# Performance work log

Hardware: AMD Instinct MI355X
Metric: run time of the kernel (lower is better)

## Reference

```python
import jax, jax.numpy as jnp
import numpy as np

D_IN = 2048
D_OUT = 2048
LN_EPS = 1e-5


def setup_inputs() -> dict:
    key = jax.random.key(0)
    kx, kw, kb = jax.random.split(key, 3)
    x = jax.random.normal(kx, (8, 2048, D_IN), dtype=jnp.float32)
    # LayerNorm affine params (torch defaults: ones / zeros)
    gamma = jnp.ones((D_IN,), dtype=jnp.float32)
    beta = jnp.zeros((D_IN,), dtype=jnp.float32)
    # weight = rand(out,in)*0.001, bias = rand(out)*0.001, alpha = ones(out)
    weight = jax.random.uniform(kw, (D_OUT, D_IN), dtype=jnp.float32) * 0.001
    bias = jax.random.uniform(kb, (D_OUT,), dtype=jnp.float32) * 0.001
    alpha = jnp.ones((D_OUT,), dtype=jnp.float32)
    return {"x": x, "gamma": gamma, "beta": beta, "weight": weight,
            "bias": bias, "alpha": alpha}


def reference(x, gamma, beta, weight, bias, alpha):
    # LayerNorm over last dim (biased variance, eps=1e-5, affine)
    mu = jnp.mean(x, axis=-1, keepdims=True)
    var = jnp.mean(jnp.square(x - mu), axis=-1, keepdims=True)
    xn = (x - mu) * jax.lax.rsqrt(var + LN_EPS) * gamma + beta
    # Binarize activations: hard sign
    a = jnp.sign(xn)
    # Binarize weights: mean-center per output row, clip, sign (STE in fwd == sign)
    centered = weight - jnp.mean(weight, axis=1, keepdims=True)  # [O, I]
    signed_w = jnp.sign(centered)
    # Linear + bias, then per-output-channel alpha scale
    out = jnp.einsum('bsi,oi->bso', a, signed_w) + bias
    return out * alpha
```

## Files before the change

kernel.cpp:

```cpp
#include <hip/hip_runtime.h>

#define DIN 2048
#define WPR 64
#define QPR 32
#define GPR 16
#define RPB 8
#define LN_EPS 1e-5f

#define GLOBAL_AS __attribute__((address_space(1)))
#define LDS_AS    __attribute__((address_space(3)))

typedef unsigned long long u64;
typedef int   i32x4  __attribute__((ext_vector_type(4)));
typedef int   i32x8  __attribute__((ext_vector_type(8)));
typedef float f32x16 __attribute__((ext_vector_type(16)));

__device__ inline float wave_sum(float v) {
    #pragma unroll
    for (int off = 32; off; off >>= 1) v += __shfl_down(v, off, 64);
    return v;
}


__global__ __launch_bounds__(256) void expand_kernel(const float* __restrict__ x,
                                                     const float* __restrict__ gamma,
                                                     const float* __restrict__ beta,
                                                     const float* __restrict__ w,
                                                     char* __restrict__ Aexp,
                                                     char* __restrict__ Bexp,
                                                     int Mblocks) {
    const int t = threadIdx.x;
    const int wid = t >> 6, lane = t & 63;
    __shared__ float red[4][2 * RPB];
    __shared__ __align__(16) unsigned stg[RPB * 256];

    const bool isA = (int)blockIdx.x < Mblocks;
    const int r0 = (isA ? (int)blockIdx.x : ((int)blockIdx.x - Mblocks)) * RPB;
    const float* src = isA ? x : w;

    float gg[8], bb[8];
    if (isA) {
        float4 g0 = ((const float4*)gamma)[t * 2];
        float4 g1 = ((const float4*)gamma)[t * 2 + 1];
        float4 b0 = ((const float4*)beta)[t * 2];
        float4 b1 = ((const float4*)beta)[t * 2 + 1];
        gg[0]=g0.x; gg[1]=g0.y; gg[2]=g0.z; gg[3]=g0.w;
        gg[4]=g1.x; gg[5]=g1.y; gg[6]=g1.z; gg[7]=g1.w;
        bb[0]=b0.x; bb[1]=b0.y; bb[2]=b0.z; bb[3]=b0.w;
        bb[4]=b1.x; bb[5]=b1.y; bb[6]=b1.z; bb[7]=b1.w;
    }

    float vv[RPB][8];
    #pragma unroll
    for (int rr = 0; rr < RPB; ++rr) {
        const float* xr = src + (size_t)(r0 + rr) * DIN;
        float4 v0 = ((const float4*)xr)[t * 2];
        float4 v1 = ((const float4*)xr)[t * 2 + 1];
        vv[rr][0]=v0.x; vv[rr][1]=v0.y; vv[rr][2]=v0.z; vv[rr][3]=v0.w;
        vv[rr][4]=v1.x; vv[rr][5]=v1.y; vv[rr][6]=v1.z; vv[rr][7]=v1.w;
    }

    #pragma unroll
    for (int rr = 0; rr < RPB; ++rr) {
        float s = 0.f, ss = 0.f;
        #pragma unroll
        for (int j = 0; j < 8; ++j) s += vv[rr][j];
        if (isA) {
            #pragma unroll
            for (int j = 0; j < 8; ++j) ss += vv[rr][j] * vv[rr][j];
        }
        s = wave_sum(s);
        if (isA) ss = wave_sum(ss);
        if (lane == 0) { red[wid][rr * 2] = s; red[wid][rr * 2 + 1] = ss; }
    }
    __syncthreads();

    #pragma unroll
    for (int rr = 0; rr < RPB; ++rr) {
        float tot = red[0][rr*2] + red[1][rr*2] + red[2][rr*2] + red[3][rr*2];
        float mu  = tot * (1.f / DIN);
        unsigned word = 0;
        if (isA) {
            float tots = red[0][rr*2+1] + red[1][rr*2+1] + red[2][rr*2+1] + red[3][rr*2+1];
            float var  = tots * (1.f / DIN) - mu * mu;
            float rs   = rsqrtf(var + LN_EPS);
            #pragma unroll
            for (int j = 0; j < 8; ++j) {
                float xn = (vv[rr][j] - mu) * rs * gg[j] + bb[j];
                word |= (xn < 0.f ? 0xAu : 0x2u) << (4 * j);
            }
        } else {
            #pragma unroll
            for (int j = 0; j < 8; ++j)
                word |= ((vv[rr][j] - mu) < 0.f ? 0xAu : 0x2u) << (4 * j);
        }
        stg[rr * 256 + (((t >> 2) ^ rr) << 2) + (t & 3)] = word;
    }
    __syncthreads();

    char* dstbase = isA ? Aexp : Bexp;
    const int bm  = r0 >> 8;
    const int rt  = (r0 >> 5) & 7;
    const int ri0 = r0 & 31;
    #pragma unroll
    for (int i2 = 0; i2 < 2; ++i2) {
        const int u  = i2 * 256 + t;
        const int sc = u >> 5;
        const int kt = (u >> 4) & 1, hb = (u >> 3) & 1, ri = u & 7;
        const int g  = sc * 4 + kt * 2 + hb;
        uint4 v = *(const uint4*)&stg[ri * 256 + ((g ^ ri) << 2)];
        const size_t doff = (((size_t)(bm * 16 + sc)) * 8 + rt) * 2048 + kt * 1024 +
                            (ri0 + ri + 32 * hb) * 16;
        *(uint4*)(dstbase + doff) = v;
    }
}

__global__ __launch_bounds__(512, 4) void fp4gemm_kernel(const char* __restrict__ Aexp,
                                                         const char* __restrict__ Bexp,
                                                         const float* __restrict__ bias,
                                                         const float* __restrict__ alpha,
                                                         float* __restrict__ out) {
    __shared__ char As[2][8192];
    __shared__ char Bs[2][16384];
    const int t = threadIdx.x;
    const int wid = t >> 6, lane = t & 63;
    const int bn = blockIdx.x & 7;
    const int bm = blockIdx.x >> 3;
    const int wr = wid >> 2;
    const int wc = wid & 3;

    const char* gA = Aexp + (size_t)(bm >> 1) * 262144 + (size_t)(bm & 1) * 8192;
    const char* gB = Bexp + (size_t)bn * 262144;

#define STAGE(BUF, S)                                                           \
    {                                                                           \
        __builtin_amdgcn_global_load_lds(                                       \
            (const GLOBAL_AS unsigned*)(gA + (size_t)(S) * 16384 + wid * 1024 + lane * 16), \
            (LDS_AS unsigned*)(&As[BUF][wid * 1024]), 16, 0, 0);                \
        __builtin_amdgcn_global_load_lds(                                       \
            (const GLOBAL_AS unsigned*)(gB + (size_t)(S) * 16384 + wid * 1024 + lane * 16), \
            (LDS_AS unsigned*)(&Bs[BUF][wid * 1024]), 16, 0, 0);                \
        __builtin_amdgcn_global_load_lds(                                       \
            (const GLOBAL_AS unsigned*)(gB + (size_t)(S) * 16384 + (wid + 8) * 1024 + lane * 16), \
            (LDS_AS unsigned*)(&Bs[BUF][(wid + 8) * 1024]), 16, 0, 0);          \
    }

    f32x16 acc[2][2];
    #pragma unroll
    for (int i = 0; i < 2; ++i)
        #pragma unroll
        for (int j = 0; j < 2; ++j)
            #pragma unroll
            for (int e = 0; e < 16; ++e) acc[i][j][e] = 0.f;

    STAGE(0, 0)
    STAGE(1, 1)
    asm volatile("s_waitcnt vmcnt(3)" ::: "memory");
    __builtin_amdgcn_s_barrier();
    asm volatile("" ::: "memory");

    #pragma unroll 1
    for (int s = 0; s < 16; ++s) {
        const int c = s & 1;
        #pragma unroll
        for (int kt = 0; kt < 2; ++kt) {
            i32x8 a[2], b[2];
            #pragma unroll
            for (int i = 0; i < 2; ++i) {
                i32x4 v = *(const i32x4*)&As[c][(wr * 2 + i) * 2048 + kt * 1024 + lane * 16];
                a[i][0]=v[0]; a[i][1]=v[1]; a[i][2]=v[2]; a[i][3]=v[3];
                a[i][4]=v[0]; a[i][5]=v[1]; a[i][6]=v[2]; a[i][7]=v[3];
            }
            #pragma unroll
            for (int j = 0; j < 2; ++j) {
                i32x4 v = *(const i32x4*)&Bs[c][(wc * 2 + j) * 2048 + kt * 1024 + lane * 16];
                b[j][0]=v[0]; b[j][1]=v[1]; b[j][2]=v[2]; b[j][3]=v[3];
                b[j][4]=v[0]; b[j][5]=v[1]; b[j][6]=v[2]; b[j][7]=v[3];
            }
            __builtin_amdgcn_s_setprio(1);
            #pragma unroll
            for (int i = 0; i < 2; ++i)
                #pragma unroll
                for (int j = 0; j < 2; ++j)
                    acc[i][j] = __builtin_amdgcn_mfma_scale_f32_32x32x64_f8f6f4(
                        a[i], b[j], acc[i][j], 4, 4,
                        0, 0x7F7F7F7F, 0, 0x7F7F7F7F);
            __builtin_amdgcn_s_setprio(0);
        }
        if (s == 15) break;
        asm volatile("s_waitcnt vmcnt(0)" ::: "memory");
        __builtin_amdgcn_s_barrier();
        asm volatile("" ::: "memory");
        if (s < 14) STAGE(c, s + 2)
    }
#undef STAGE

    const int cl = lane & 31;
    const int rb = 4 * (lane >> 5);
    #pragma unroll
    for (int i = 0; i < 2; ++i) {
        #pragma unroll
        for (int j = 0; j < 2; ++j) {
            const int col = bn * 256 + (wc * 2 + j) * 32 + cl;
            const float bi = bias[col], al = alpha[col];
            const int row0 = bm * 128 + (wr * 2 + i) * 32 + rb;
            #pragma unroll
            for (int reg = 0; reg < 16; ++reg) {
                const int row = row0 + (reg & 3) + 8 * (reg >> 2);
                out[(size_t)row * 2048 + col] = (acc[i][j][reg] + bi) * al;
            }
        }
    }
}

__global__ __launch_bounds__(256) void w_pack_kernel(const float* __restrict__ w,
                                                     unsigned* __restrict__ wpk) {
    const int row = blockIdx.x;
    const int t = threadIdx.x;
    const float* wr = w + (size_t)row * DIN;
    float4 v0 = ((const float4*)wr)[t * 2];
    float4 v1 = ((const float4*)wr)[t * 2 + 1];
    float s = v0.x + v0.y + v0.z + v0.w + v1.x + v1.y + v1.z + v1.w;

    __shared__ float red[4];
    float wsum = wave_sum(s);
    int wid = t >> 6, lane = t & 63;
    if (lane == 0) red[wid] = wsum;
    __syncthreads();
    float mu = (red[0] + red[1] + red[2] + red[3]) * (1.f / DIN);

    float vv[8] = {v0.x, v0.y, v0.z, v0.w, v1.x, v1.y, v1.z, v1.w};
    unsigned byte = 0;
    #pragma unroll
    for (int j = 0; j < 8; ++j)
        byte |= ((vv[j] - mu) < 0.f ? 1u : 0u) << j;

    __shared__ unsigned char bytes[256];
    bytes[t] = (unsigned char)byte;
    __syncthreads();
    if (t < 64) {
        unsigned wd = (unsigned)bytes[t * 4] | ((unsigned)bytes[t * 4 + 1] << 8) |
                      ((unsigned)bytes[t * 4 + 2] << 16) | ((unsigned)bytes[t * 4 + 3] << 24);
        wpk[(size_t)row * WPR + t] = wd;
    }
}

__global__ __launch_bounds__(256) void ln_pack_kernel(const float* __restrict__ x,
                                                      const float* __restrict__ gamma,
                                                      const float* __restrict__ beta,
                                                      unsigned* __restrict__ apk) {
    const int row = blockIdx.x;
    const int t = threadIdx.x;
    const float* xr = x + (size_t)row * DIN;
    float4 v0 = ((const float4*)xr)[t * 2];
    float4 v1 = ((const float4*)xr)[t * 2 + 1];
    float s  = v0.x + v0.y + v0.z + v0.w + v1.x + v1.y + v1.z + v1.w;
    float ss = v0.x * v0.x + v0.y * v0.y + v0.z * v0.z + v0.w * v0.w +
               v1.x * v1.x + v1.y * v1.y + v1.z * v1.z + v1.w * v1.w;

    __shared__ float red[8];
    float wsum = wave_sum(s), wssum = wave_sum(ss);
    int wid = t >> 6, lane = t & 63;
    if (lane == 0) { red[wid] = wsum; red[4 + wid] = wssum; }
    __syncthreads();
    float tot  = red[0] + red[1] + red[2] + red[3];
    float tots = red[4] + red[5] + red[6] + red[7];
    float mu  = tot * (1.f / DIN);
    float var = tots * (1.f / DIN) - mu * mu;
    float rs  = rsqrtf(var + LN_EPS);

    float4 g0 = ((const float4*)gamma)[t * 2];
    float4 g1 = ((const float4*)gamma)[t * 2 + 1];
    float4 b0 = ((const float4*)beta)[t * 2];
    float4 b1 = ((const float4*)beta)[t * 2 + 1];
    float vv[8] = {v0.x, v0.y, v0.z, v0.w, v1.x, v1.y, v1.z, v1.w};
    float gg[8] = {g0.x, g0.y, g0.z, g0.w, g1.x, g1.y, g1.z, g1.w};
    float bb[8] = {b0.x, b0.y, b0.z, b0.w, b1.x, b1.y, b1.z, b1.w};
    unsigned byte = 0;
    #pragma unroll
    for (int j = 0; j < 8; ++j) {
        float xn = (vv[j] - mu) * rs * gg[j] + bb[j];
        byte |= (xn < 0.f ? 1u : 0u) << j;
    }

    __shared__ unsigned char bytes[256];
    bytes[t] = (unsigned char)byte;
    __syncthreads();
    if (t < 64) {
        unsigned wd = (unsigned)bytes[t * 4] | ((unsigned)bytes[t * 4 + 1] << 8) |
                      ((unsigned)bytes[t * 4 + 2] << 16) | ((unsigned)bytes[t * 4 + 3] << 24);
        apk[(size_t)row * WPR + t] = wd;
    }
}

__global__ __launch_bounds__(256) void bingemm_kernel(const u64* __restrict__ A,
                                                      const u64* __restrict__ B,
                                                      const float* __restrict__ bias,
                                                      const float* __restrict__ alpha,
                                                      float* __restrict__ out) {
    __shared__ u64 S[2 * 128 * QPR];
    uint4* Sg = (uint4*)S;
    const int t = threadIdx.x;
    const int bn = blockIdx.x, bm = blockIdx.y;

    const uint4* Ag = (const uint4*)(A + (size_t)bm * 128 * QPR);
    #pragma unroll
    for (int i = 0; i < 8; ++i) {
        int id = t + i * 256;
        int row = id >> 4, g = id & 15;
        Sg[(row << 4) + (g ^ (row & 15))] = Ag[id];
    }
    const uint4* Bg = (const uint4*)(B + (size_t)bn * 128 * QPR);
    #pragma unroll
    for (int i = 0; i < 8; ++i) {
        int id = t + i * 256;
        int row = id >> 4, g = id & 15;
        Sg[2048 + (row << 4) + (g ^ (row & 15))] = Bg[id];
    }
    __syncthreads();

    const int tr = t >> 4;
    const int tc = t & 15;
    const ulonglong2* Sq = (const ulonglong2*)S;
    const int abase = tr * GPR;
    const int bbase = 2048 + tc * GPR;

    int acc[8][8] = {};
    u64 a0[8][2], b0[8][2], a1[8][2], b1[8][2];

#define LOADK(KK, AR, BR)                                            \
    {                                                                \
        const int ka = abase + ((KK) ^ tr);                          \
        const int kb = bbase + ((KK) ^ tc);                          \
        _Pragma("unroll")                                            \
        for (int r = 0; r < 8; ++r) {                                \
            ulonglong2 v = Sq[ka + r * 256];                         \
            AR[r][0] = v.x; AR[r][1] = v.y;                          \
        }                                                            \
        _Pragma("unroll")                                            \
        for (int c2 = 0; c2 < 8; ++c2) {                             \
            ulonglong2 v = Sq[kb + c2 * 256];                        \
            BR[c2][0] = v.x; BR[c2][1] = v.y;                        \
        }                                                            \
    }

#define COMPK(AR, BR)                                                \
    {                                                                \
        _Pragma("unroll")                                            \
        for (int r = 0; r < 8; ++r) {                                \
            _Pragma("unroll")                                        \
            for (int c2 = 0; c2 < 8; ++c2) {                         \
                acc[r][c2] += __popcll(AR[r][0] ^ BR[c2][0]);        \
                acc[r][c2] += __popcll(AR[r][1] ^ BR[c2][1]);        \
            }                                                        \
        }                                                            \
    }

    LOADK(0, a0, b0);
    #pragma unroll 1
    for (int kk = 0; kk < 14; kk += 2) {
        LOADK(kk + 1, a1, b1);
        COMPK(a0, b0);
        LOADK(kk + 2, a0, b0);
        COMPK(a1, b1);
    }
    LOADK(15, a1, b1);
    COMPK(a0, b0);
    COMPK(a1, b1);
#undef LOADK
#undef COMPK

    float bi[8], al[8];
    #pragma unroll
    for (int c2 = 0; c2 < 8; ++c2) {
        int col = bn * 128 + tc + 16 * c2;
        bi[c2] = bias[col];
        al[c2] = alpha[col];
    }
    #pragma unroll
    for (int r = 0; r < 8; ++r) {
        const size_t row = (size_t)bm * 128 + tr + 16 * r;
        float* op = out + row * 2048 + bn * 128 + tc;
        #pragma unroll
        for (int c2 = 0; c2 < 8; ++c2)
            op[16 * c2] = ((float)(DIN - 2 * acc[r][c2]) + bi[c2]) * al[c2];
    }
}

extern "C" void kernel_launch(void* const* d_in, const int* in_sizes, int n_in,
                              void* d_out, int out_size, void* d_ws, size_t ws_size,
                              hipStream_t stream) {
    const float* x     = (const float*)d_in[0];
    const float* gamma = (const float*)d_in[1];
    const float* beta  = (const float*)d_in[2];
    const float* w     = (const float*)d_in[3];
    const float* bias  = (const float*)d_in[4];
    const float* alpha = (const float*)d_in[5];
    float* out = (float*)d_out;

    const int M = in_sizes[0] / DIN;
    const int N = in_sizes[3] / DIN;

    const size_t needA = (size_t)M * (DIN / 2);
    const size_t needB = (size_t)N * (DIN / 2);

    if (ws_size >= needA + needB && (M % 256) == 0 && (N % 256) == 0) {
        char* Aexp = (char*)d_ws;
        char* Bexp = (char*)d_ws + needA;
        expand_kernel<<<(M + N) / RPB, 256, 0, stream>>>(x, gamma, beta, w,
                                                         Aexp, Bexp, M / RPB);
        dim3 grid((N / 256) * (M / 128));
        fp4gemm_kernel<<<grid, 512, 0, stream>>>(Aexp, Bexp, bias, alpha, out);
    } else {
        unsigned* apk = (unsigned*)d_ws;
        unsigned* wpk = (unsigned*)((char*)d_ws + (size_t)M * WPR * 4);
        w_pack_kernel<<<N, 256, 0, stream>>>(w, wpk);
        ln_pack_kernel<<<M, 256, 0, stream>>>(x, gamma, beta, apk);
        dim3 grid(N / 128, M / 128);
        bingemm_kernel<<<grid, 256, 0, stream>>>((const u64*)apk, (const u64*)wpk,
                                                 bias, alpha, out);
    }
}
```

Baseline: 89.65 us.

## Load GEMM fragments directly into registers with double buffering, dropping LDS staging

```diff
diff --git a/kernel.cpp b/kernel.cpp
--- a/kernel.cpp
+++ b/kernel.cpp
@@ -115,99 +115,105 @@
     }
 }
 
-__global__ __launch_bounds__(512, 4) void fp4gemm_kernel(const char* __restrict__ Aexp,
+__global__ __launch_bounds__(256, 2) void fp4gemm_kernel(const char* __restrict__ Aexp,
                                                          const char* __restrict__ Bexp,
                                                          const float* __restrict__ bias,
                                                          const float* __restrict__ alpha,
-                                                         float* __restrict__ out) {
-    __shared__ char As[2][8192];
-    __shared__ char Bs[2][16384];
+                                                         float* __restrict__ out,
+                                                         int ldc, int nRb, int nCg) {
     const int t = threadIdx.x;
-    const int wid = t >> 6, lane = t & 63;
-    const int bn = blockIdx.x & 7;
-    const int bm = blockIdx.x >> 3;
-    const int wr = wid >> 2;
-    const int wc = wid & 3;
-
-    const char* gA = Aexp + (size_t)(bm >> 1) * 262144 + (size_t)(bm & 1) * 8192;
-    const char* gB = Bexp + (size_t)bn * 262144;
-
-#define STAGE(BUF, S)                                                           \
-    {                                                                           \
-        __builtin_amdgcn_global_load_lds(                                       \
-            (const GLOBAL_AS unsigned*)(gA + (size_t)(S) * 16384 + wid * 1024 + lane * 16), \
-            (LDS_AS unsigned*)(&As[BUF][wid * 1024]), 16, 0, 0);                \
-        __builtin_amdgcn_global_load_lds(                                       \
-            (const GLOBAL_AS unsigned*)(gB + (size_t)(S) * 16384 + wid * 1024 + lane * 16), \
-            (LDS_AS unsigned*)(&Bs[BUF][wid * 1024]), 16, 0, 0);                \
-        __builtin_amdgcn_global_load_lds(                                       \
-            (const GLOBAL_AS unsigned*)(gB + (size_t)(S) * 16384 + (wid + 8) * 1024 + lane * 16), \
-            (LDS_AS unsigned*)(&Bs[BUF][(wid + 8) * 1024]), 16, 0, 0);          \
-    }
-
-    f32x16 acc[2][2];
-    #pragma unroll
-    for (int i = 0; i < 2; ++i)
+    const int wv = t >> 6, lane = t & 63;
+    const int bid = blockIdx.x;
+    const int q = bid >> 3;
+    const int hi = q / nRb;
+    const int blockR = q - hi * nRb;
+    const int blockC = (bid & 7) * nCg + hi;
+
+    const int wr = wv >> 1, wc = wv & 1;
+    const int r128 = blockR * 2 + wr;
+    const int c64  = blockC * 2 + wc;
+    const int bm = r128 >> 1, rtbase = (r128 & 1) * 4;
+    const int bn = c64 >> 2,  ctbase = (c64 & 3) * 2;
+
+    const char* aP = Aexp + (size_t)bm * 262144 + (size_t)rtbase * 2048 + lane * 16;
+    const char* bP = Bexp + (size_t)bn * 262144 + (size_t)ctbase * 2048 + lane * 16;
+
+#define LOADP(P, AR, BR)                                                     \
+    {                                                                        \
+        const size_t off = (size_t)(((P) >> 1) * 16384 + ((P) & 1) * 1024);  \
+        _Pragma("unroll")                                                    \
+        for (int i = 0; i < 4; ++i)                                          \
+            AR[i] = *(const i32x4*)(aP + off + i * 2048);                    \
+        _Pragma("unroll")                                                    \
+        for (int j = 0; j < 2; ++j)                                          \
+            BR[j] = *(const i32x4*)(bP + off + j * 2048);                    \
+    }
+
+#define COMP(AR, BR)                                                         \
+    {                                                                        \
+        i32x8 aa[4], bb2[2];                                                 \
+        _Pragma("unroll")                                                    \
+        for (int i = 0; i < 4; ++i) {                                        \
+            aa[i][0]=AR[i][0]; aa[i][1]=AR[i][1];                            \
+            aa[i][2]=AR[i][2]; aa[i][3]=AR[i][3];                            \
+            aa[i][4]=AR[i][0]; aa[i][5]=AR[i][1];                            \
+            aa[i][6]=AR[i][2]; aa[i][7]=AR[i][3];                            \
+        }                                                                    \
+        _Pragma("unroll")                                                    \
+        for (int j = 0; j < 2; ++j) {                                        \
+            bb2[j][0]=BR[j][0]; bb2[j][1]=BR[j][1];                          \
+            bb2[j][2]=BR[j][2]; bb2[j][3]=BR[j][3];                          \
+            bb2[j][4]=BR[j][0]; bb2[j][5]=BR[j][1];                          \
+            bb2[j][6]=BR[j][2]; bb2[j][7]=BR[j][3];                          \
+        }                                                                    \
+        __builtin_amdgcn_s_setprio(1);                                       \
+        _Pragma("unroll")                                                    \
+        for (int i = 0; i < 4; ++i)                                          \
+            _Pragma("unroll")                                                \
+            for (int j = 0; j < 2; ++j)                                      \
+                acc[i][j] = __builtin_amdgcn_mfma_scale_f32_32x32x64_f8f6f4( \
+                    aa[i], bb2[j], acc[i][j], 4, 4,                          \
+                    0, 0x7F7F7F7F, 0, 0x7F7F7F7F);                           \
+        __builtin_amdgcn_s_setprio(0);                                       \
+    }
+
+    f32x16 acc[4][2];
+    #pragma unroll
+    for (int i = 0; i < 4; ++i)
         #pragma unroll
         for (int j = 0; j < 2; ++j)
             #pragma unroll
             for (int e = 0; e < 16; ++e) acc[i][j][e] = 0.f;
 
-    STAGE(0, 0)
-    STAGE(1, 1)
-    asm volatile("s_waitcnt vmcnt(3)" ::: "memory");
-    __builtin_amdgcn_s_barrier();
-    asm volatile("" ::: "memory");
-
+    i32x4 a0[4], b0[2], a1[4], b1[2];
+
+    LOADP(0, a0, b0);
     #pragma unroll 1
-    for (int s = 0; s < 16; ++s) {
-        const int c = s & 1;
-        #pragma unroll
-        for (int kt = 0; kt < 2; ++kt) {
-            i32x8 a[2], b[2];
-            #pragma unroll
-            for (int i = 0; i < 2; ++i) {
-                i32x4 v = *(const i32x4*)&As[c][(wr * 2 + i) * 2048 + kt * 1024 + lane * 16];
-                a[i][0]=v[0]; a[i][1]=v[1]; a[i][2]=v[2]; a[i][3]=v[3];
-                a[i][4]=v[0]; a[i][5]=v[1]; a[i][6]=v[2]; a[i][7]=v[3];
-            }
-            #pragma unroll
-            for (int j = 0; j < 2; ++j) {
-                i32x4 v = *(const i32x4*)&Bs[c][(wc * 2 + j) * 2048 + kt * 1024 + lane * 16];
-                b[j][0]=v[0]; b[j][1]=v[1]; b[j][2]=v[2]; b[j][3]=v[3];
-                b[j][4]=v[0]; b[j][5]=v[1]; b[j][6]=v[2]; b[j][7]=v[3];
-            }
-            __builtin_amdgcn_s_setprio(1);
-            #pragma unroll
-            for (int i = 0; i < 2; ++i)
-                #pragma unroll
-                for (int j = 0; j < 2; ++j)
-                    acc[i][j] = __builtin_amdgcn_mfma_scale_f32_32x32x64_f8f6f4(
-                        a[i], b[j], acc[i][j], 4, 4,
-                        0, 0x7F7F7F7F, 0, 0x7F7F7F7F);
-            __builtin_amdgcn_s_setprio(0);
-        }
-        if (s == 15) break;
-        asm volatile("s_waitcnt vmcnt(0)" ::: "memory");
-        __builtin_amdgcn_s_barrier();
-        asm volatile("" ::: "memory");
-        if (s < 14) STAGE(c, s + 2)
-    }
-#undef STAGE
+    for (int p = 0; p < 30; p += 2) {
+        LOADP(p + 1, a1, b1);
+        COMP(a0, b0);
+        LOADP(p + 2, a0, b0);
+        COMP(a1, b1);
+    }
+    LOADP(31, a1, b1);
+    COMP(a0, b0);
+    COMP(a1, b1);
+#undef LOADP
+#undef COMP
 
     const int cl = lane & 31;
     const int rb = 4 * (lane >> 5);
     #pragma unroll
-    for (int i = 0; i < 2; ++i) {
+    for (int i = 0; i < 4; ++i) {
         #pragma unroll
         for (int j = 0; j < 2; ++j) {
-            const int col = bn * 256 + (wc * 2 + j) * 32 + cl;
+            const int col = bn * 256 + (ctbase + j) * 32 + cl;
             const float bi = bias[col], al = alpha[col];
-            const int row0 = bm * 128 + (wr * 2 + i) * 32 + rb;
+            const int row0 = bm * 256 + (rtbase + i) * 32 + rb;
             #pragma unroll
             for (int reg = 0; reg < 16; ++reg) {
                 const int row = row0 + (reg & 3) + 8 * (reg >> 2);
-                out[(size_t)row * 2048 + col] = (acc[i][j][reg] + bi) * al;
+                out[(size_t)row * ldc + col] = (acc[i][j][reg] + bi) * al;
             }
         }
     }
@@ -404,13 +410,16 @@
     const size_t needA = (size_t)M * (DIN / 2);
     const size_t needB = (size_t)N * (DIN / 2);
 
-    if (ws_size >= needA + needB && (M % 256) == 0 && (N % 256) == 0) {
+    if (ws_size >= needA + needB && (M % 256) == 0 && (N % 1024) == 0) {
         char* Aexp = (char*)d_ws;
         char* Bexp = (char*)d_ws + needA;
         expand_kernel<<<(M + N) / RPB, 256, 0, stream>>>(x, gamma, beta, w,
                                                          Aexp, Bexp, M / RPB);
-        dim3 grid((N / 256) * (M / 128));
-        fp4gemm_kernel<<<grid, 512, 0, stream>>>(Aexp, Bexp, bias, alpha, out);
+        const int nRb = M / 256;
+        const int nCg = (N / 128) / 8;
+        const int nblocks = nRb * (N / 128);
+        fp4gemm_kernel<<<nblocks, 256, 0, stream>>>(Aexp, Bexp, bias, alpha, out,
+                                                    N, nRb, nCg);
     } else {
         unsigned* apk = (unsigned*)d_ws;
         unsigned* wpk = (unsigned*)((char*)d_ws + (size_t)M * WPR * 4);
```

Measured after the change: 97.98 us. 1.09x slower.

## Shrink GEMM tile to 128x128, triple-buffer LDS, and XCD-aware block mapping

Applied to the files above, without the earlier changes.

```diff
diff --git a/kernel.cpp b/kernel.cpp
--- a/kernel.cpp
+++ b/kernel.cpp
@@ -115,34 +115,38 @@
     }
 }
 
-__global__ __launch_bounds__(512, 4) void fp4gemm_kernel(const char* __restrict__ Aexp,
+__global__ __launch_bounds__(256, 3) void fp4gemm_kernel(const char* __restrict__ Aexp,
                                                          const char* __restrict__ Bexp,
                                                          const float* __restrict__ bias,
                                                          const float* __restrict__ alpha,
-                                                         float* __restrict__ out) {
-    __shared__ char As[2][8192];
-    __shared__ char Bs[2][16384];
+                                                         float* __restrict__ out,
+                                                         int ldc, int nBm, int nCgX) {
+    __shared__ char As[3][8192];
+    __shared__ char Bs[3][8192];
     const int t = threadIdx.x;
-    const int wid = t >> 6, lane = t & 63;
-    const int bn = blockIdx.x & 7;
-    const int bm = blockIdx.x >> 3;
-    const int wr = wid >> 2;
-    const int wc = wid & 3;
-
-    const char* gA = Aexp + (size_t)(bm >> 1) * 262144 + (size_t)(bm & 1) * 8192;
-    const char* gB = Bexp + (size_t)bn * 262144;
+    const int wv = t >> 6, lane = t & 63;
+    const int xcd = blockIdx.x & 7;
+    const int g   = blockIdx.x >> 3;
+    const int bm128 = g % nBm;
+    const int bn128 = xcd * nCgX + g / nBm;
+
+    const int wr = wv >> 1, wc = wv & 1;
+
+    const char* gA = Aexp + (size_t)(bm128 >> 1) * 262144 + (size_t)(bm128 & 1) * 8192;
+    const char* gB = Bexp + (size_t)(bn128 >> 1) * 262144 + (size_t)(bn128 & 1) * 8192;
 
 #define STAGE(BUF, S)                                                           \
     {                                                                           \
-        __builtin_amdgcn_global_load_lds(                                       \
-            (const GLOBAL_AS unsigned*)(gA + (size_t)(S) * 16384 + wid * 1024 + lane * 16), \
-            (LDS_AS unsigned*)(&As[BUF][wid * 1024]), 16, 0, 0);                \
-        __builtin_amdgcn_global_load_lds(                                       \
-            (const GLOBAL_AS unsigned*)(gB + (size_t)(S) * 16384 + wid * 1024 + lane * 16), \
-            (LDS_AS unsigned*)(&Bs[BUF][wid * 1024]), 16, 0, 0);                \
-        __builtin_amdgcn_global_load_lds(                                       \
-            (const GLOBAL_AS unsigned*)(gB + (size_t)(S) * 16384 + (wid + 8) * 1024 + lane * 16), \
-            (LDS_AS unsigned*)(&Bs[BUF][(wid + 8) * 1024]), 16, 0, 0);          \
+        _Pragma("unroll")                                                       \
+        for (int i2 = 0; i2 < 2; ++i2) {                                        \
+            const int ch = wv * 2 + i2;                                         \
+            __builtin_amdgcn_global_load_lds(                                   \
+                (const GLOBAL_AS unsigned*)(gA + (size_t)(S) * 16384 + ch * 1024 + lane * 16), \
+                (LDS_AS unsigned*)(&As[BUF][ch * 1024]), 16, 0, 0);             \
+            __builtin_amdgcn_global_load_lds(                                   \
+                (const GLOBAL_AS unsigned*)(gB + (size_t)(S) * 16384 + ch * 1024 + lane * 16), \
+                (LDS_AS unsigned*)(&Bs[BUF][ch * 1024]), 16, 0, 0);             \
+        }                                                                       \
     }
 
     f32x16 acc[2][2];
@@ -155,27 +159,33 @@
 
     STAGE(0, 0)
     STAGE(1, 1)
-    asm volatile("s_waitcnt vmcnt(3)" ::: "memory");
+    asm volatile("s_waitcnt vmcnt(4)" ::: "memory");
     __builtin_amdgcn_s_barrier();
     asm volatile("" ::: "memory");
 
+    int c = 0;
     #pragma unroll 1
     for (int s = 0; s < 16; ++s) {
-        const int c = s & 1;
+        if (s <= 13) {
+            const int nb = (c == 0) ? 2 : c - 1;
+            STAGE(nb, s + 2)
+        }
         #pragma unroll
         for (int kt = 0; kt < 2; ++kt) {
-            i32x8 a[2], b[2];
+            i32x4 a[2], b[2];
+            #pragma unroll
+            for (int i = 0; i < 2; ++i)
+                a[i] = *(const i32x4*)&As[c][(wr * 2 + i) * 2048 + kt * 1024 + lane * 16];
+            #pragma unroll
+            for (int j = 0; j < 2; ++j)
+                b[j] = *(const i32x4*)&Bs[c][(wc * 2 + j) * 2048 + kt * 1024 + lane * 16];
+            i32x8 aa[2], bb2[2];
             #pragma unroll
             for (int i = 0; i < 2; ++i) {
-                i32x4 v = *(const i32x4*)&As[c][(wr * 2 + i) * 2048 + kt * 1024 + lane * 16];
-                a[i][0]=v[0]; a[i][1]=v[1]; a[i][2]=v[2]; a[i][3]=v[3];
-                a[i][4]=v[0]; a[i][5]=v[1]; a[i][6]=v[2]; a[i][7]=v[3];
-            }
-            #pragma unroll
-            for (int j = 0; j < 2; ++j) {
-                i32x4 v = *(const i32x4*)&Bs[c][(wc * 2 + j) * 2048 + kt * 1024 + lane * 16];
-                b[j][0]=v[0]; b[j][1]=v[1]; b[j][2]=v[2]; b[j][3]=v[3];
-                b[j][4]=v[0]; b[j][5]=v[1]; b[j][6]=v[2]; b[j][7]=v[3];
+                aa[i][0]=a[i][0]; aa[i][1]=a[i][1]; aa[i][2]=a[i][2]; aa[i][3]=a[i][3];
+                aa[i][4]=a[i][0]; aa[i][5]=a[i][1]; aa[i][6]=a[i][2]; aa[i][7]=a[i][3];
+                bb2[i][0]=b[i][0]; bb2[i][1]=b[i][1]; bb2[i][2]=b[i][2]; bb2[i][3]=b[i][3];
+                bb2[i][4]=b[i][0]; bb2[i][5]=b[i][1]; bb2[i][6]=b[i][2]; bb2[i][7]=b[i][3];
             }
             __builtin_amdgcn_s_setprio(1);
             #pragma unroll
@@ -183,15 +193,16 @@
                 #pragma unroll
                 for (int j = 0; j < 2; ++j)
                     acc[i][j] = __builtin_amdgcn_mfma_scale_f32_32x32x64_f8f6f4(
-                        a[i], b[j], acc[i][j], 4, 4,
+                        aa[i], bb2[j], acc[i][j], 4, 4,
                         0, 0x7F7F7F7F, 0, 0x7F7F7F7F);
             __builtin_amdgcn_s_setprio(0);
         }
         if (s == 15) break;
-        asm volatile("s_waitcnt vmcnt(0)" ::: "memory");
+        if (s <= 13) { asm volatile("s_waitcnt vmcnt(4)" ::: "memory"); }
+        else         { asm volatile("s_waitcnt vmcnt(0)" ::: "memory"); }
         __builtin_amdgcn_s_barrier();
         asm volatile("" ::: "memory");
-        if (s < 14) STAGE(c, s + 2)
+        c = (c == 2) ? 0 : c + 1;
     }
 #undef STAGE
 
@@ -201,13 +212,13 @@
     for (int i = 0; i < 2; ++i) {
         #pragma unroll
         for (int j = 0; j < 2; ++j) {
-            const int col = bn * 256 + (wc * 2 + j) * 32 + cl;
+            const int col = bn128 * 128 + (wc * 2 + j) * 32 + cl;
             const float bi = bias[col], al = alpha[col];
-            const int row0 = bm * 128 + (wr * 2 + i) * 32 + rb;
+            const int row0 = bm128 * 128 + (wr * 2 + i) * 32 + rb;
             #pragma unroll
             for (int reg = 0; reg < 16; ++reg) {
                 const int row = row0 + (reg & 3) + 8 * (reg >> 2);
-                out[(size_t)row * 2048 + col] = (acc[i][j][reg] + bi) * al;
+                out[(size_t)row * ldc + col] = (acc[i][j][reg] + bi) * al;
             }
         }
     }
@@ -404,13 +415,16 @@
     const size_t needA = (size_t)M * (DIN / 2);
     const size_t needB = (size_t)N * (DIN / 2);
 
-    if (ws_size >= needA + needB && (M % 256) == 0 && (N % 256) == 0) {
+    if (ws_size >= needA + needB && (M % 256) == 0 && (N % 1024) == 0) {
         char* Aexp = (char*)d_ws;
         char* Bexp = (char*)d_ws + needA;
         expand_kernel<<<(M + N) / RPB, 256, 0, stream>>>(x, gamma, beta, w,
                                                          Aexp, Bexp, M / RPB);
-        dim3 grid((N / 256) * (M / 128));
-        fp4gemm_kernel<<<grid, 512, 0, stream>>>(Aexp, Bexp, bias, alpha, out);
+        const int nBm = M / 128;
+        const int nCgX = (N / 128) / 8;
+        const int nblocks = nBm * (N / 128);
+        fp4gemm_kernel<<<nblocks, 256, 0, stream>>>(Aexp, Bexp, bias, alpha, out,
+                                                    N, nBm, nCgX);
     } else {
         unsigned* apk = (unsigned*)d_ws;
         unsigned* wpk = (unsigned*)((char*)d_ws + (size_t)M * WPR * 4);
```

Measured after the change: 103.2 us. 15.1% more time.
